# Performance work log

Hardware: AMD Instinct MI355X
Metric: run time of the kernel (lower is better)

Reference implementation:

```python
import jax, jax.numpy as jnp
import numpy as np

N = 150000   # nonempty octree nodes at this depth
CIN = 256
CB = 64      # bottleneck channels = out_channels / bottleneck
COUT = 256
G = 32       # group-norm groups
K = 27       # 3x3x3 neighborhood
EPS = 1e-5


def group_norm(x, gamma, beta, groups=G):
    # x: [N, C]; octree GN treats the N nodes as the spatial extent of one instance
    n, c = x.shape
    xg = x.reshape(n, groups, c // groups)
    mu = xg.mean(axis=(0, 2), keepdims=True)
    var = xg.var(axis=(0, 2), keepdims=True)
    xg = (xg - mu) * jax.lax.rsqrt(var + EPS)
    return xg.reshape(n, c) * gamma + beta


def setup_inputs() -> dict:
    key = jax.random.key(0)
    ks = jax.random.split(key, 5)
    return {
        "data": jax.random.normal(ks[0], (N, CIN), jnp.float32),
        "neigh": jax.random.randint(ks[1], (N, K), 0, N, jnp.int32),
        "w1a": jax.random.normal(ks[2], (CIN, CB), jnp.float32) * 0.05,
        "g1a": jnp.ones((CB,), jnp.float32),
        "b1a": jnp.zeros((CB,), jnp.float32),
        "w3": jax.random.normal(ks[3], (K, CB, CB), jnp.float32) * 0.05,
        "g3": jnp.ones((CB,), jnp.float32),
        "b3": jnp.zeros((CB,), jnp.float32),
        "w1b": jax.random.normal(ks[4], (CB, COUT), jnp.float32) * 0.05,
        "g1b": jnp.ones((COUT,), jnp.float32),
        "b1b": jnp.zeros((COUT,), jnp.float32),
    }


def reference(data, neigh, w1a, g1a, b1a, w3, g3, b3, w1b, g1b, b1b):
    # conv1x1a + GN + ReLU
    x = jax.nn.relu(group_norm(data @ w1a, g1a, b1a))
    # octree 3x3x3 sparse conv: gather 27 neighbors, GEMM against [27,CB,CB] kernel
    gathered = x[neigh]                      # [N, 27, CB]
    y = jnp.einsum('nkc,kcd->nd', gathered, w3)
    y = jax.nn.relu(group_norm(y, g3, b3))
    # conv1x1b + GN
    z = group_norm(y @ w1b, g1b, b1b)
    # residual add (in_channels == out_channels -> identity skip) + ReLU
    return jax.nn.relu(z + data)
```

## Files before the change

### kernel.cpp

```cpp
#include <hip/hip_runtime.h>
#include <math.h>

#define CIN 256
#define CB 64
#define COUT 256
#define KNB 27
#define EPS 1e-5f

typedef unsigned short u16;
typedef __attribute__((ext_vector_type(8))) short short8;
typedef __attribute__((ext_vector_type(4))) float f32x4;

__device__ inline short f2bf(float f) {
    union { float f; unsigned u; } v; v.f = f;
    unsigned r = v.u + 0x7fff + ((v.u >> 16) & 1);
    return (short)(r >> 16);
}
__device__ inline float bf2f(short s) {
    union { unsigned u; float f; } v; v.u = ((unsigned)(u16)s) << 16;
    return v.f;
}
__device__ inline short8 pack8(float4 x0, float4 x1) {
    short8 r;
    r[0] = f2bf(x0.x); r[1] = f2bf(x0.y); r[2] = f2bf(x0.z); r[3] = f2bf(x0.w);
    r[4] = f2bf(x1.x); r[5] = f2bf(x1.y); r[6] = f2bf(x1.z); r[7] = f2bf(x1.w);
    return r;
}

__global__ void k_prep(const float* __restrict__ w1a, const float* __restrict__ w3,
                       const float* __restrict__ w1b, u16* __restrict__ w1at,
                       u16* __restrict__ w3img, u16* __restrict__ w1bt)
{
    int i = blockIdx.x * 256 + threadIdx.x;
    if (i < 16384) {
        int k = i >> 6, d = i & 63;
        w1at[d * 256 + k] = (u16)f2bf(w1a[i]);
    } else if (i < 126976) {
        int j = i - 16384;
        int k = j >> 12, c = (j >> 6) & 63, d = j & 63;
        w3img[(size_t)k * 4096 + d * 64 + (c ^ ((d & 7) << 3))] = (u16)f2bf(w3[j]);
    } else if (i < 143360) {
        int j = i - 126976;
        int c = j >> 8, d = j & 255;
        w1bt[d * 64 + c] = (u16)f2bf(w1b[j]);
    }
}

__global__ __launch_bounds__(256) void k_gemm1(const float* __restrict__ data,
        const u16* __restrict__ w1at, u16* __restrict__ t1,
        float* __restrict__ stats, int n)
{
    __shared__ float s_sum[32], s_sq[32];
    const int tid = threadIdx.x;
    if (tid < 32) { s_sum[tid] = 0.f; s_sq[tid] = 0.f; }
    __syncthreads();
    const int l = tid & 63, wv = tid >> 6;
    const int ll = l & 15, lh = l >> 4;
    const int rowbase = blockIdx.x * 256 + wv * 64;

    f32x4 acc[4][4] = {};
#pragma unroll
    for (int kc = 0; kc < 8; ++kc) {
        short8 b[4];
#pragma unroll
        for (int f = 0; f < 4; ++f)
            b[f] = *(const short8*)(w1at + (size_t)(f * 16 + ll) * 256 + kc * 32 + lh * 8);
#pragma unroll
        for (int rt = 0; rt < 4; ++rt) {
            int row = rowbase + rt * 16 + ll;
            int rowc = (row < n) ? row : 0;
            const float* ar = data + (size_t)rowc * CIN + kc * 32 + lh * 8;
            short8 a = pack8(*(const float4*)ar, *(const float4*)(ar + 4));
#pragma unroll
            for (int f = 0; f < 4; ++f)
                acc[rt][f] = __builtin_amdgcn_mfma_f32_16x16x32_bf16(a, b[f], acc[rt][f], 0, 0, 0);
        }
    }
    float gs[4] = {0.f, 0.f, 0.f, 0.f}, gq[4] = {0.f, 0.f, 0.f, 0.f};
#pragma unroll
    for (int rt = 0; rt < 4; ++rt) {
#pragma unroll
        for (int f = 0; f < 4; ++f) {
#pragma unroll
            for (int r = 0; r < 4; ++r) {
                int rr = rowbase + rt * 16 + lh * 4 + r;
                if (rr < n) {
                    float v = acc[rt][f][r];
                    t1[(size_t)rr * CB + f * 16 + ll] = (u16)f2bf(v);
                    gs[f] += v; gq[f] += v * v;
                }
            }
        }
    }
#pragma unroll
    for (int f = 0; f < 4; ++f) {
        float s = gs[f], q = gq[f];
        s += __shfl_xor(s, 1); s += __shfl_xor(s, 16); s += __shfl_xor(s, 32);
        q += __shfl_xor(q, 1); q += __shfl_xor(q, 16); q += __shfl_xor(q, 32);
        if ((l & 0x31) == 0) {
            atomicAdd(&s_sum[f * 8 + (ll >> 1)], s);
            atomicAdd(&s_sq [f * 8 + (ll >> 1)], q);
        }
    }
    __syncthreads();
    if (tid < 32) {
        atomicAdd(&stats[tid], s_sum[tid]);
        atomicAdd(&stats[32 + tid], s_sq[tid]);
    }
}

__global__ void k_apply64(u16* __restrict__ buf, const float* __restrict__ st,
        const float* __restrict__ gamma, const float* __restrict__ beta, int n)
{
    const float cnt = (float)n * 2.0f;
    const int total = n * 8;
    for (int i = blockIdx.x * blockDim.x + threadIdx.x; i < total;
         i += gridDim.x * blockDim.x) {
        int c0 = (i & 7) * 8;
        short8 v = ((short8*)buf)[i];
#pragma unroll
        for (int j = 0; j < 8; ++j) {
            int c = c0 + j, g = c >> 1;
            float mu = st[g] / cnt;
            float var = st[32 + g] / cnt - mu * mu;
            float inv = rsqrtf(var + EPS);
            float x = bf2f(v[j]);
            x = fmaxf((x - mu) * inv * gamma[c] + beta[c], 0.f);
            v[j] = f2bf(x);
        }
        ((short8*)buf)[i] = v;
    }
}

__global__ __launch_bounds__(256) void k_conv(const u16* __restrict__ xb,
        const int* __restrict__ neigh, const u16* __restrict__ w3img,
        u16* __restrict__ y, float* __restrict__ stats, int n)
{
    __shared__ u16 s_w3[2][4096];
    __shared__ float s_sum[32], s_sq[32];
    const int tid = threadIdx.x;
    if (tid < 32) { s_sum[tid] = 0.f; s_sq[tid] = 0.f; }
    const int row0 = blockIdx.x * 64;
    const int l = tid & 63, wv = tid >> 6;
    const int ll = l & 15, lh = l >> 4;
    const int myrow = row0 + wv * 16 + ll;
    const int rowc = (myrow < n) ? myrow : 0;
    const int* __restrict__ nrow = neigh + (size_t)rowc * KNB;

    {
        const short8* src = (const short8*)(w3img);
        short8 v0 = src[tid * 2], v1 = src[tid * 2 + 1];
        ((short8*)&s_w3[0][0])[tid * 2] = v0;
        ((short8*)&s_w3[0][0])[tid * 2 + 1] = v1;
    }
    int idx0 = nrow[0];
    int idxn = nrow[1];
    __syncthreads();
    short8 a0c, a1c;
    {
        const u16* xr = xb + (size_t)idx0 * CB + lh * 8;
        a0c = *(const short8*)(xr);
        a1c = *(const short8*)(xr + 32);
    }

    f32x4 acc[4] = {};
    for (int k = 0; k < KNB; ++k) {
        const int cur = k & 1;
        const bool more = (k + 1 < KNB);
        int idx2 = 0;
        short8 w0, w1, a0n, a1n;
        if (k + 2 < KNB) idx2 = nrow[k + 2];
        if (more) {
            const short8* src = (const short8*)(w3img + (size_t)(k + 1) * 4096);
            w0 = src[tid * 2];
            w1 = src[tid * 2 + 1];
            const u16* xr = xb + (size_t)idxn * CB + lh * 8;
            a0n = *(const short8*)(xr);
            a1n = *(const short8*)(xr + 32);
        }
#pragma unroll
        for (int f = 0; f < 4; ++f) {
            int d = f * 16 + ll;
            int swz = (d & 7) << 4;
            short8 b0 = *(const short8*)((const char*)&s_w3[cur][0] + d * 128 + ((lh * 16) ^ swz));
            short8 b1 = *(const short8*)((const char*)&s_w3[cur][0] + d * 128 + ((64 + lh * 16) ^ swz));
            acc[f] = __builtin_amdgcn_mfma_f32_16x16x32_bf16(a0c, b0, acc[f], 0, 0, 0);
            acc[f] = __builtin_amdgcn_mfma_f32_16x16x32_bf16(a1c, b1, acc[f], 0, 0, 0);
        }
        if (more) {
            ((short8*)&s_w3[cur ^ 1][0])[tid * 2] = w0;
            ((short8*)&s_w3[cur ^ 1][0])[tid * 2 + 1] = w1;
            a0c = a0n; a1c = a1n; idxn = idx2;
        }
        __syncthreads();
    }
    float gs[4] = {0.f, 0.f, 0.f, 0.f}, gq[4] = {0.f, 0.f, 0.f, 0.f};
#pragma unroll
    for (int f = 0; f < 4; ++f) {
#pragma unroll
        for (int r = 0; r < 4; ++r) {
            int rr = row0 + wv * 16 + lh * 4 + r;
            if (rr < n) {
                float v = acc[f][r];
                y[(size_t)rr * CB + f * 16 + ll] = (u16)f2bf(v);
                gs[f] += v; gq[f] += v * v;
            }
        }
    }
#pragma unroll
    for (int f = 0; f < 4; ++f) {
        float s = gs[f], q = gq[f];
        s += __shfl_xor(s, 1); s += __shfl_xor(s, 16); s += __shfl_xor(s, 32);
        q += __shfl_xor(q, 1); q += __shfl_xor(q, 16); q += __shfl_xor(q, 32);
        if ((l & 0x31) == 0) {
            atomicAdd(&s_sum[f * 8 + (ll >> 1)], s);
            atomicAdd(&s_sq [f * 8 + (ll >> 1)], q);
        }
    }
    __syncthreads();
    if (tid < 32) {
        atomicAdd(&stats[64 + tid], s_sum[tid]);
        atomicAdd(&stats[96 + tid], s_sq[tid]);
    }
}

__global__ __launch_bounds__(256) void k_gemm2(const u16* __restrict__ y2,
        const u16* __restrict__ w1bt, float* __restrict__ z, u16* __restrict__ zb,
        float* __restrict__ stats, const float* __restrict__ g3,
        const float* __restrict__ b3, int n)
{
    __shared__ float s_sum[8], s_sq[8];
    const int tid = threadIdx.x;
    if (tid < 8) { s_sum[tid] = 0.f; s_sq[tid] = 0.f; }
    __syncthreads();
    const int l = tid & 63, wv = tid >> 6;
    const int ll = l & 15, lh = l >> 4;
    const int rowbase = blockIdx.x * 256 + wv * 64;
    const int cb = blockIdx.y;

    const float* st2 = stats + 64;
    const float cnt2 = (float)n * 2.0f;
    float sc[16], sh[16];
#pragma unroll
    for (int j = 0; j < 16; ++j) {
        int c = (j < 8) ? (lh * 8 + j) : (32 + lh * 8 + (j - 8));
        int g = c >> 1;
        float mu = st2[g] / cnt2;
        float var = st2[32 + g] / cnt2 - mu * mu;
        float inv = rsqrtf(var + EPS);
        float gm = g3[c];
        sc[j] = inv * gm;
        sh[j] = b3[c] - mu * inv * gm;
    }

    short8 b0[4], b1[4];
#pragma unroll
    for (int f = 0; f < 4; ++f) {
        const u16* br = w1bt + (size_t)(cb * 64 + f * 16 + ll) * CB + lh * 8;
        b0[f] = *(const short8*)(br);
        b1[f] = *(const short8*)(br + 32);
    }
    f32x4 acc[4][4] = {};
#pragma unroll
    for (int rt = 0; rt < 4; ++rt) {
        int row = rowbase + rt * 16 + ll;
        int rowc = (row < n) ? row : 0;
        const u16* ar = y2 + (size_t)rowc * CB + lh * 8;
        short8 r0 = *(const short8*)(ar);
        short8 r1 = *(const short8*)(ar + 32);
        short8 a0, a1;
#pragma unroll
        for (int j = 0; j < 8; ++j) {
            a0[j] = f2bf(fmaxf(bf2f(r0[j]) * sc[j] + sh[j], 0.f));
            a1[j] = f2bf(fmaxf(bf2f(r1[j]) * sc[8 + j] + sh[8 + j], 0.f));
        }
#pragma unroll
        for (int f = 0; f < 4; ++f) {
            acc[rt][f] = __builtin_amdgcn_mfma_f32_16x16x32_bf16(a0, b0[f], acc[rt][f], 0, 0, 0);
            acc[rt][f] = __builtin_amdgcn_mfma_f32_16x16x32_bf16(a1, b1[f], acc[rt][f], 0, 0, 0);
        }
    }
    float gs[4] = {0.f, 0.f, 0.f, 0.f}, gq[4] = {0.f, 0.f, 0.f, 0.f};
#pragma unroll
    for (int rt = 0; rt < 4; ++rt) {
#pragma unroll
        for (int f = 0; f < 4; ++f) {
#pragma unroll
            for (int r = 0; r < 4; ++r) {
                int rr = rowbase + rt * 16 + lh * 4 + r;
                if (rr < n) {
                    float v = acc[rt][f][r];
                    size_t off = (size_t)rr * COUT + cb * 64 + f * 16 + ll;
                    if (zb) zb[off] = (u16)f2bf(v); else z[off] = v;
                    gs[f] += v; gq[f] += v * v;
                }
            }
        }
    }
#pragma unroll
    for (int f = 0; f < 4; ++f) {
        float s = gs[f], q = gq[f];
        s += __shfl_xor(s, 1); s += __shfl_xor(s, 2); s += __shfl_xor(s, 4);
        s += __shfl_xor(s, 16); s += __shfl_xor(s, 32);
        q += __shfl_xor(q, 1); q += __shfl_xor(q, 2); q += __shfl_xor(q, 4);
        q += __shfl_xor(q, 16); q += __shfl_xor(q, 32);
        if ((l & 0x37) == 0) {
            atomicAdd(&s_sum[f * 2 + (ll >> 3)], s);
            atomicAdd(&s_sq [f * 2 + (ll >> 3)], q);
        }
    }
    __syncthreads();
    if (tid < 8) {
        atomicAdd(&stats[128 + cb * 8 + tid], s_sum[tid]);
        atomicAdd(&stats[160 + cb * 8 + tid], s_sq[tid]);
    }
}

__global__ void k_final_bf(float* __restrict__ out, const u16* __restrict__ zb,
        const float* __restrict__ data, const float* __restrict__ st,
        const float* __restrict__ gamma, const float* __restrict__ beta, int n)
{
    const float cnt = (float)n * 8.0f;
    const int total = n * 32;
    for (int i = blockIdx.x * blockDim.x + threadIdx.x; i < total;
         i += gridDim.x * blockDim.x) {
        int c0 = (i & 31) * 8;
        int g = c0 >> 3;
        float mu = st[g] / cnt;
        float var = st[32 + g] / cnt - mu * mu;
        float inv = rsqrtf(var + EPS);
        short8 zv = ((const short8*)zb)[i];
        float dd[8], oo[8];
        *(float4*)dd = *(const float4*)(data + (size_t)i * 8);
        *(float4*)(dd + 4) = *(const float4*)(data + (size_t)i * 8 + 4);
#pragma unroll
        for (int j = 0; j < 8; ++j)
            oo[j] = fmaxf((bf2f(zv[j]) - mu) * inv * gamma[c0 + j] + beta[c0 + j] + dd[j], 0.f);
        *(float4*)(out + (size_t)i * 8) = *(float4*)oo;
        *(float4*)(out + (size_t)i * 8 + 4) = *(float4*)(oo + 4);
    }
}

__global__ void k_final(float* __restrict__ zo, const float* __restrict__ data,
        const float* __restrict__ st, const float* __restrict__ gamma,
        const float* __restrict__ beta, int n)
{
    const float cnt = (float)n * 8.0f;
    const int total = n * (COUT / 4);
    for (int i = blockIdx.x * blockDim.x + threadIdx.x; i < total;
         i += gridDim.x * blockDim.x) {
        int c4 = (i & (COUT / 4 - 1)) * 4;
        int g = c4 >> 3;
        float mu = st[g] / cnt;
        float var = st[32 + g] / cnt - mu * mu;
        float inv = rsqrtf(var + EPS);
        float4 zv = *(float4*)(zo + (size_t)i * 4);
        float4 dv = *(const float4*)(data + (size_t)i * 4);
        zv.x = fmaxf((zv.x - mu) * inv * gamma[c4 + 0] + beta[c4 + 0] + dv.x, 0.f);
        zv.y = fmaxf((zv.y - mu) * inv * gamma[c4 + 1] + beta[c4 + 1] + dv.y, 0.f);
        zv.z = fmaxf((zv.z - mu) * inv * gamma[c4 + 2] + beta[c4 + 2] + dv.z, 0.f);
        zv.w = fmaxf((zv.w - mu) * inv * gamma[c4 + 3] + beta[c4 + 3] + dv.w, 0.f);
        *(float4*)(zo + (size_t)i * 4) = zv;
    }
}

extern "C" void kernel_launch(void* const* d_in, const int* in_sizes, int n_in,
                              void* d_out, int out_size, void* d_ws, size_t ws_size,
                              hipStream_t stream)
{
    const float* data = (const float*)d_in[0];
    const int*   neigh = (const int*)d_in[1];
    const float* w1a = (const float*)d_in[2];
    const float* g1a = (const float*)d_in[3];
    const float* b1a = (const float*)d_in[4];
    const float* w3  = (const float*)d_in[5];
    const float* g3  = (const float*)d_in[6];
    const float* b3  = (const float*)d_in[7];
    const float* w1b = (const float*)d_in[8];
    const float* g1b = (const float*)d_in[9];
    const float* b1b = (const float*)d_in[10];
    float* out = (float*)d_out;
    float* ws  = (float*)d_ws;

    const int n = in_sizes[0] / CIN;

    float* stats = ws;
    u16* w1at  = (u16*)(ws + 256);
    u16* w3img = w1at + 16384;
    u16* w1bt  = w3img + 110592;
    u16* t1    = w1bt + 16384;
    u16* ybuf  = t1 + (size_t)n * CB;
    u16* zb    = nullptr;
    {
        size_t need = 1024 + 286720 + (size_t)n * CB * 4 + (size_t)n * COUT * 2;
        if (ws_size >= need) zb = ybuf + (size_t)n * CB;
    }

    hipMemsetAsync(stats, 0, 192 * sizeof(float), stream);

    const int nb64  = (n + 63) / 64;
    const int nb256 = (n + 255) / 256;
    k_prep<<<560, 256, 0, stream>>>(w1a, w3, w1b, w1at, w3img, w1bt);
    k_gemm1<<<nb256, 256, 0, stream>>>(data, w1at, t1, stats, n);
    k_apply64<<<2048, 256, 0, stream>>>(t1, stats, g1a, b1a, n);
    k_conv<<<nb64, 256, 0, stream>>>(t1, neigh, w3img, ybuf, stats, n);
    k_gemm2<<<dim3(nb256, 4), 256, 0, stream>>>(ybuf, w1bt, out, zb, stats, g3, b3, n);
    if (zb)
        k_final_bf<<<2048, 256, 0, stream>>>(out, zb, data, stats + 128, g1b, b1b, n);
    else
        k_final<<<2048, 256, 0, stream>>>(out, data, stats + 128, g1b, b1b, n);
}
```

Before: 296.1 us.

## Double rows per conv block and stream weights via global_load_lds

Result: no change. 292.6 us (-1.2%).

```diff
diff --git a/kernel.cpp b/kernel.cpp
--- a/kernel.cpp
+++ b/kernel.cpp
@@ -10,6 +10,11 @@
 typedef unsigned short u16;
 typedef __attribute__((ext_vector_type(8))) short short8;
 typedef __attribute__((ext_vector_type(4))) float f32x4;
+
+typedef const __attribute__((address_space(1))) unsigned int* gas_u32p;
+typedef __attribute__((address_space(3))) unsigned int* las_u32p;
+#define GLL(g, p) __builtin_amdgcn_global_load_lds((gas_u32p)(const void*)(g), \
+        (las_u32p)(void*)(p), 16, 0, 0)
 
 __device__ inline short f2bf(float f) {
     union { float f; unsigned u; } v; v.f = f;
@@ -140,70 +145,81 @@
     __shared__ float s_sum[32], s_sq[32];
     const int tid = threadIdx.x;
     if (tid < 32) { s_sum[tid] = 0.f; s_sq[tid] = 0.f; }
-    const int row0 = blockIdx.x * 64;
+    const int row0 = blockIdx.x * 128;
     const int l = tid & 63, wv = tid >> 6;
     const int ll = l & 15, lh = l >> 4;
-    const int myrow = row0 + wv * 16 + ll;
-    const int rowc = (myrow < n) ? myrow : 0;
-    const int* __restrict__ nrow = neigh + (size_t)rowc * KNB;
-
+    const int r0 = row0 + wv * 32 + ll;
+    const int r1 = r0 + 16;
+    const int r0c = (r0 < n) ? r0 : 0;
+    const int r1c = (r1 < n) ? r1 : 0;
+    const int* __restrict__ nrow0 = neigh + (size_t)r0c * KNB;
+    const int* __restrict__ nrow1 = neigh + (size_t)r1c * KNB;
+
+    u16* ld0 = &s_w3[0][0] + wv * 1024 + l * 8;
+    u16* ld1 = &s_w3[1][0] + wv * 1024 + l * 8;
+    const u16* gw = w3img + wv * 1024 + l * 8;
+
+    GLL(gw, ld0);
+    GLL(gw + 512, ld0 + 512);
+    int ia = nrow0[0], ib = nrow1[0];
     {
-        const short8* src = (const short8*)(w3img);
-        short8 v0 = src[tid * 2], v1 = src[tid * 2 + 1];
-        ((short8*)&s_w3[0][0])[tid * 2] = v0;
-        ((short8*)&s_w3[0][0])[tid * 2 + 1] = v1;
-    }
-    int idx0 = nrow[0];
-    int idxn = nrow[1];
-    __syncthreads();
-    short8 a0c, a1c;
+        const u16* xa = xb + (size_t)ia * CB + lh * 8;
+        const u16* xc = xb + (size_t)ib * CB + lh * 8;
+        ia = nrow0[1]; ib = nrow1[1];
+        __builtin_amdgcn_sched_barrier(0);
+    }
+    short8 a0c, a1c, a2c, a3c;
     {
-        const u16* xr = xb + (size_t)idx0 * CB + lh * 8;
-        a0c = *(const short8*)(xr);
-        a1c = *(const short8*)(xr + 32);
-    }
-
-    f32x4 acc[4] = {};
+        const u16* xa = xb + (size_t)nrow0[0] * CB + lh * 8;
+        const u16* xc = xb + (size_t)nrow1[0] * CB + lh * 8;
+        a0c = *(const short8*)xa; a1c = *(const short8*)(xa + 32);
+        a2c = *(const short8*)xc; a3c = *(const short8*)(xc + 32);
+    }
+    __syncthreads();
+
+    f32x4 acc[2][4] = {};
     for (int k = 0; k < KNB; ++k) {
         const int cur = k & 1;
-        const bool more = (k + 1 < KNB);
-        int idx2 = 0;
-        short8 w0, w1, a0n, a1n;
-        if (k + 2 < KNB) idx2 = nrow[k + 2];
-        if (more) {
-            const short8* src = (const short8*)(w3img + (size_t)(k + 1) * 4096);
-            w0 = src[tid * 2];
-            w1 = src[tid * 2 + 1];
-            const u16* xr = xb + (size_t)idxn * CB + lh * 8;
-            a0n = *(const short8*)(xr);
-            a1n = *(const short8*)(xr + 32);
-        }
+        short8 a0n, a1n, a2n, a3n;
+        if (k + 1 < KNB) {
+            const u16* gsrc = w3img + (size_t)(k + 1) * 4096 + wv * 1024 + l * 8;
+            u16* ldst = cur ? ld0 : ld1;
+            GLL(gsrc, ldst);
+            GLL(gsrc + 512, ldst + 512);
+            int i2 = nrow0[k + 1], i3 = nrow1[k + 1];
+            const u16* xa = xb + (size_t)i2 * CB + lh * 8;
+            const u16* xc = xb + (size_t)i3 * CB + lh * 8;
+            a0n = *(const short8*)xa; a1n = *(const short8*)(xa + 32);
+            a2n = *(const short8*)xc; a3n = *(const short8*)(xc + 32);
+        }
+        __builtin_amdgcn_sched_barrier(0);
 #pragma unroll
         for (int f = 0; f < 4; ++f) {
             int d = f * 16 + ll;
             int swz = (d & 7) << 4;
             short8 b0 = *(const short8*)((const char*)&s_w3[cur][0] + d * 128 + ((lh * 16) ^ swz));
             short8 b1 = *(const short8*)((const char*)&s_w3[cur][0] + d * 128 + ((64 + lh * 16) ^ swz));
-            acc[f] = __builtin_amdgcn_mfma_f32_16x16x32_bf16(a0c, b0, acc[f], 0, 0, 0);
-            acc[f] = __builtin_amdgcn_mfma_f32_16x16x32_bf16(a1c, b1, acc[f], 0, 0, 0);
-        }
-        if (more) {
-            ((short8*)&s_w3[cur ^ 1][0])[tid * 2] = w0;
-            ((short8*)&s_w3[cur ^ 1][0])[tid * 2 + 1] = w1;
-            a0c = a0n; a1c = a1n; idxn = idx2;
-        }
+            acc[0][f] = __builtin_amdgcn_mfma_f32_16x16x32_bf16(a0c, b0, acc[0][f], 0, 0, 0);
+            acc[0][f] = __builtin_amdgcn_mfma_f32_16x16x32_bf16(a1c, b1, acc[0][f], 0, 0, 0);
+            acc[1][f] = __builtin_amdgcn_mfma_f32_16x16x32_bf16(a2c, b0, acc[1][f], 0, 0, 0);
+            acc[1][f] = __builtin_amdgcn_mfma_f32_16x16x32_bf16(a3c, b1, acc[1][f], 0, 0, 0);
+        }
+        if (k + 1 < KNB) { a0c = a0n; a1c = a1n; a2c = a2n; a3c = a3n; }
         __syncthreads();
     }
     float gs[4] = {0.f, 0.f, 0.f, 0.f}, gq[4] = {0.f, 0.f, 0.f, 0.f};
 #pragma unroll
-    for (int f = 0; f < 4; ++f) {
-#pragma unroll
-        for (int r = 0; r < 4; ++r) {
-            int rr = row0 + wv * 16 + lh * 4 + r;
-            if (rr < n) {
-                float v = acc[f][r];
-                y[(size_t)rr * CB + f * 16 + ll] = (u16)f2bf(v);
-                gs[f] += v; gq[f] += v * v;
+    for (int rt = 0; rt < 2; ++rt) {
+#pragma unroll
+        for (int f = 0; f < 4; ++f) {
+#pragma unroll
+            for (int r = 0; r < 4; ++r) {
+                int rr = row0 + wv * 32 + rt * 16 + lh * 4 + r;
+                if (rr < n) {
+                    float v = acc[rt][f][r];
+                    y[(size_t)rr * CB + f * 16 + ll] = (u16)f2bf(v);
+                    gs[f] += v; gq[f] += v * v;
+                }
             }
         }
     }
@@ -398,12 +414,12 @@
 
     hipMemsetAsync(stats, 0, 192 * sizeof(float), stream);
 
-    const int nb64  = (n + 63) / 64;
+    const int nb128 = (n + 127) / 128;
     const int nb256 = (n + 255) / 256;
     k_prep<<<560, 256, 0, stream>>>(w1a, w3, w1b, w1at, w3img, w1bt);
     k_gemm1<<<nb256, 256, 0, stream>>>(data, w1at, t1, stats, n);
     k_apply64<<<2048, 256, 0, stream>>>(t1, stats, g1a, b1a, n);
-    k_conv<<<nb64, 256, 0, stream>>>(t1, neigh, w3img, ybuf, stats, n);
+    k_conv<<<nb128, 256, 0, stream>>>(t1, neigh, w3img, ybuf, stats, n);
     k_gemm2<<<dim3(nb256, 4), 256, 0, stream>>>(ybuf, w1bt, out, zb, stats, g3, b3, n);
     if (zb)
         k_final_bf<<<2048, 256, 0, stream>>>(out, zb, data, stats + 128, g1b, b1b, n);
```
